# Kernel tuning notes

Measured on AMD Instinct MI355X. Metric: run time of the kernel, lower is better.

## Reference

```python
import jax, jax.numpy as jnp
import numpy as np

K = 3          # kernel_size
PAD = 1        # padding
FOCAL = 50.0
DMIN = 1.0
DMAX = 50.0
ORIG_H = 512.0  # original_image_size[1]


def setup_inputs() -> dict:
    key = jax.random.key(0)
    k1, k2 = jax.random.split(key)
    x = jax.random.normal(k1, (4, 64, 256, 256), dtype=jnp.float32)
    # conv weight [out_ch, in_ch, K, K] (bias=False)
    W = jax.random.normal(k2, (64, 64, K, K), dtype=jnp.float32) * 0.05
    return {"x": x, "W": W}


def _bilinear(img, xs, ys):
    """Bilinear sample img [B,C,H,W] at float pixel coords xs, ys [B,Ho,Wo].
    Zero padding outside the image (grid_sample semantics)."""
    B, C, H, Wd = img.shape
    Ho, Wo = xs.shape[1], xs.shape[2]
    x0 = jnp.floor(xs); y0 = jnp.floor(ys)
    wx1 = xs - x0; wx0 = 1.0 - wx1
    wy1 = ys - y0; wy0 = 1.0 - wy1
    img_flat = img.reshape(B, C, H * Wd)

    def gat(ix, iy):
        ixi = ix.astype(jnp.int32); iyi = iy.astype(jnp.int32)
        valid = (ixi >= 0) & (ixi < Wd) & (iyi >= 0) & (iyi < H)
        idx = jnp.clip(iyi, 0, H - 1) * Wd + jnp.clip(ixi, 0, Wd - 1)
        v = jnp.take_along_axis(img_flat, idx.reshape(B, 1, Ho * Wo), axis=2)
        v = v.reshape(B, C, Ho, Wo)
        return v * valid[:, None].astype(img.dtype)

    return (gat(x0, y0) * (wx0 * wy0)[:, None]
            + gat(x0 + 1, y0) * (wx1 * wy0)[:, None]
            + gat(x0, y0 + 1) * (wx0 * wy1)[:, None]
            + gat(x0 + 1, y0 + 1) * (wx1 * wy1)[:, None])


def reference(x, W):
    B, C, H, Wd = x.shape
    downsample = ORIG_H / H  # 2.0 for H=256

    # upper branch: plain 3x3 conv, padding 1, no bias
    x_upper = jax.lax.conv_general_dilated(x, W, (1, 1), [(PAD, PAD), (PAD, PAD)])

    # geometry -> clamped depth (geometry_method='max', formulation='depth')
    depth = jnp.clip(jnp.max(x, axis=1), DMIN, DMAX)  # [B,H,W]

    # Frontal homography: Hom01 = I with [1,2] = focal/(downsample*depth);
    # its inverse Hom10 shifts y by -s.
    s = FOCAL / (downsample * depth)  # [B,H,W]

    xi = jnp.arange(Wd, dtype=x.dtype)[None, None, :]
    yi = jnp.arange(H, dtype=x.dtype)[None, :, None]
    xs = jnp.broadcast_to(xi, (B, H, Wd))
    ys = yi - s  # Hom10 applied to pixel coords

    # warp input with per-pixel Hom10 (pass_warped_images=True)
    x2 = _bilinear(x, xs, ys)

    # deformable conv: per-pixel offset from Hom10 is (dx,dy)=(0,-s) for all 9 taps
    x_lower = jnp.zeros_like(x_upper)
    for ky in range(K):
        for kx in range(K):
            sx = xs + (kx - PAD)
            sy = ys + (ky - PAD)
            tap = _bilinear(x2, sx, sy)  # [B,C,H,W]
            x_lower = x_lower + jnp.einsum('bchw,oc->bohw', tap, W[:, :, ky, kx])

    # project with 'min' over the stacked (upper, lower) branches
    return jnp.minimum(x_upper, x_lower)
```

## Files before the change

kernel.cpp:

```cpp
#include <hip/hip_runtime.h>
#include <cmath>

constexpr int BB = 4, CC = 64, HH = 256, WW = 256;
constexpr int WP = 258;
constexpr int C2R = 257;

typedef short short8 __attribute__((ext_vector_type(8)));
typedef float f32x4 __attribute__((ext_vector_type(4)));
#define MFMA_BF16 __builtin_amdgcn_mfma_f32_16x16x32_bf16

union U16x8 { uint4 v; unsigned short h[8]; };
union U16x4 { uint2 v; unsigned short h[4]; };

__device__ inline unsigned short f2bf(float f) {
  unsigned u = __builtin_bit_cast(unsigned, f);
  u += 0x7fffu + ((u >> 16) & 1u);
  return (unsigned short)(u >> 16);
}
__device__ inline unsigned short f2bf_trunc(float f) {
  return (unsigned short)(__builtin_bit_cast(unsigned, f) >> 16);
}
__device__ inline float bf2f(unsigned short h) {
  unsigned u = ((unsigned)h) << 16;
  return __builtin_bit_cast(float, u);
}

__global__ __launch_bounds__(256, 4) void k_pack(const float* __restrict__ x,
                                                 float* __restrict__ s,
                                                 unsigned short* __restrict__ xn) {
  __shared__ float tile[CC * 129];
  __shared__ float pmax[2][128];
  const int t = threadIdx.x;
  const int half = blockIdx.x & 1, y = blockIdx.x >> 1, b = blockIdx.y;
  const int px0 = half * 128;
  const int pxl = t & 127, chb = (t >> 7) * 32;

  const float* base = x + (size_t)b * CC * HH * WW + (size_t)y * WW + px0 + pxl;
  float m = -1e30f;
#pragma unroll 8
  for (int i = 0; i < 32; ++i) {
    float v = base[(size_t)(chb + i) * HH * WW];
    tile[(chb + i) * 129 + pxl] = v;
    m = fmaxf(m, v);
  }
  pmax[t >> 7][pxl] = m;

  uint4* xn4 = (uint4*)xn;
  if (t < 8) {
    int col = half ? (WP - 1) : 0;
    xn4[(((size_t)(b * HH + y) * WP + col) * CC + t * 8) >> 3] =
        make_uint4(0, 0, 0, 0);
  }
  __syncthreads();

  if (t < 128) {
    float mm = fmaxf(pmax[0][t], pmax[1][t]);
    s[(b * HH + y) * WW + px0 + t] = 25.0f / fminf(fmaxf(mm, 1.0f), 50.0f);
  }
#pragma unroll
  for (int g = 0; g < 4; ++g) {
    int px = g * 32 + (t >> 3), c8 = t & 7;
    U16x8 r;
#pragma unroll
    for (int j = 0; j < 8; ++j) r.h[j] = f2bf(tile[(c8 * 8 + j) * 129 + px]);
    xn4[(((size_t)(b * HH + y) * WP + px0 + px + 1) * CC + c8 * 8) >> 3] = r.v;
  }
}

__global__ __launch_bounds__(256) void k_wpack(const float* __restrict__ Wt,
                                               unsigned short* __restrict__ Wp) {
  int gid = blockIdx.x * 256 + threadIdx.x;
  int lane = gid & 63, kc = (gid >> 6) & 1, mt = (gid >> 7) & 3, tap = gid >> 9;
  int o = mt * 16 + (lane & 15);
  int kb = kc * 32 + (lane >> 4) * 8;
  int ky = tap / 3, kx = tap % 3;
  U16x8 r;
#pragma unroll
  for (int j = 0; j < 8; ++j)
    r.h[j] = f2bf(Wt[o * 576 + (kb + j) * 9 + ky * 3 + kx]);
  ((uint4*)Wp)[gid] = r.v;
}

__global__ __launch_bounds__(256, 4) void k_lower(const unsigned short* __restrict__ xn,
                                                  const unsigned short* __restrict__ Wp,
                                                  const float* __restrict__ s,
                                                  unsigned short* __restrict__ c2) {
  __shared__ uint4 lds[2112];
  const int t = threadIdx.x;
  const int ctile = blockIdx.x & 3, tr = blockIdx.x >> 2;
  const int b = blockIdx.y;
  const int r0 = tr * 2 - 1;
  const int colBase = ctile * 64;

  const uint4* xn4 = (const uint4*)xn;
#pragma unroll 1
  for (int g = 0; g < 3; ++g) {
    float w0a[3], w1a[3];
    int o0a[3], o1a[3], la[3];
    bool act[3], va[3];
#pragma unroll
    for (int j = 0; j < 3; ++j) {
      int idx = (g * 3 + j) * 256 + t;
      act[j] = idx < 2112;
      int rr_ = idx / 528, rem = idx % 528;
      int col_ = rem >> 3, ch_ = rem & 7;
      int xrow = r0 - 1 + rr_;
      va[j] = act[j] && (xrow >= 0) && (xrow < HH);
      la[j] = (rr_ * 66 + col_) * 8 + (ch_ ^ (col_ & 7));
      float sv = 0.0f;
      int pxc = min(max(colBase + col_ - 1, 0), WW - 1);
      if (va[j]) sv = s[(b * HH + min(max(xrow, 0), HH - 1)) * WW + pxc];
      float ys = (float)xrow - sv;
      float fy = floorf(ys);
      float wfr = ys - fy;
      int i0 = (int)fy;
      w0a[j] = (i0 >= 0) ? 1.0f - wfr : 0.0f;
      w1a[j] = (i0 + 1 >= 0) ? wfr : 0.0f;
      int a0 = min(max(i0, 0), HH - 1), a1 = min(max(i0 + 1, 0), HH - 1);
      o0a[j] = ((b * HH + a0) * WP + colBase + col_) * 8 + ch_;
      o1a[j] = ((b * HH + a1) * WP + colBase + col_) * 8 + ch_;
    }
#pragma unroll
    for (int j = 0; j < 3; ++j) {
      if (act[j]) {
        uint4 v = make_uint4(0, 0, 0, 0);
        if (va[j]) {
          U16x8 u0, u1, rr;
          u0.v = xn4[o0a[j]];
          u1.v = xn4[o1a[j]];
#pragma unroll
          for (int k = 0; k < 8; ++k)
            rr.h[k] = f2bf_trunc(w0a[j] * bf2f(u0.h[k]) + w1a[j] * bf2f(u1.h[k]));
          v = rr.v;
        }
        lds[la[j]] = v;
      }
    }
  }

  const int lane = t & 63, w = t >> 6;
  const int ow = w & 1, ch2 = w >> 1;
  const int quad = lane >> 4, l15 = lane & 15;
  const uint4* wp4 = (const uint4*)Wp;
  __syncthreads();

  f32x4 acc[2][2][2];
#pragma unroll
  for (int pt = 0; pt < 2; ++pt)
#pragma unroll
    for (int rr = 0; rr < 2; ++rr)
#pragma unroll
      for (int ct = 0; ct < 2; ++ct) acc[pt][rr][ct] = {0.f, 0.f, 0.f, 0.f};

#pragma unroll 1
  for (int kc = 0; kc < 2; ++kc) {
    short8 wf[9][2];
#pragma unroll
    for (int tap = 0; tap < 9; ++tap)
#pragma unroll
      for (int ct = 0; ct < 2; ++ct)
        wf[tap][ct] = __builtin_bit_cast(
            short8, wp4[((tap * 4 + (ow * 2 + ct)) * 2 + kc) * 64 + lane]);
#pragma unroll
    for (int pt = 0; pt < 2; ++pt) {
#pragma unroll
      for (int ir = 0; ir < 4; ++ir) {
#pragma unroll
        for (int kx = 0; kx < 3; ++kx) {
          int col = ch2 * 32 + pt * 16 + l15 + kx;
          short8 xf = __builtin_bit_cast(
              short8, lds[(ir * 66 + col) * 8 + ((kc * 4 + quad) ^ (col & 7))]);
          if (ir <= 2) {
#pragma unroll
            for (int ct = 0; ct < 2; ++ct)
              acc[pt][0][ct] = MFMA_BF16(wf[ir * 3 + kx][ct], xf, acc[pt][0][ct], 0, 0, 0);
          }
          if (ir >= 1) {
#pragma unroll
            for (int ct = 0; ct < 2; ++ct)
              acc[pt][1][ct] = MFMA_BF16(wf[(ir - 1) * 3 + kx][ct], xf, acc[pt][1][ct], 0, 0, 0);
          }
        }
      }
    }
  }

  uint2* c2u = (uint2*)c2;
#pragma unroll
  for (int pt = 0; pt < 2; ++pt) {
    int px = colBase + ch2 * 32 + pt * 16 + l15;
#pragma unroll
    for (int rr = 0; rr < 2; ++rr) {
      int r = r0 + rr;
      if (r > 255) continue;
#pragma unroll
      for (int ct = 0; ct < 2; ++ct) {
        f32x4 A = acc[pt][rr][ct];
        int og = (ow * 2 + ct) * 4 + quad;
        unsigned short h0 = f2bf(A[0]), h1 = f2bf(A[1]), h2 = f2bf(A[2]), h3 = f2bf(A[3]);
        uint2 val = make_uint2((unsigned)h0 | ((unsigned)h1 << 16),
                               (unsigned)h2 | ((unsigned)h3 << 16));
        c2u[(size_t)((b * 16 + og) * C2R + (r + 1)) * WW + px] = val;
      }
    }
  }
}

__global__ __launch_bounds__(256, 4) void k_final(const unsigned short* __restrict__ xn,
                                                  const unsigned short* __restrict__ Wp,
                                                  const float* __restrict__ s,
                                                  const unsigned short* __restrict__ c2,
                                                  float* __restrict__ out) {
  __shared__ uint4 lds[2112];
  const int t = threadIdx.x;
  const int ctile = blockIdx.x & 3, tr = blockIdx.x >> 2;
  const int b = blockIdx.y;
  const int y0 = tr * 2;
  const int colBase = ctile * 64;

  const uint4* src4 = (const uint4*)xn;
#pragma unroll 1
  for (int i = 0; i < 9; ++i) {
    int idx = i * 256 + t;
    if (idx < 2112) {
      int rr_ = idx / 528, rem = idx % 528;
      int col_ = rem >> 3, ch_ = rem & 7;
      int xrow = y0 - 1 + rr_;
      uint4 v = make_uint4(0, 0, 0, 0);
      if (xrow >= 0 && xrow < HH)
        v = src4[((size_t)(b * HH + xrow) * WP + colBase + col_) * 8 + ch_];
      lds[(rr_ * 66 + col_) * 8 + (ch_ ^ (col_ & 7))] = v;
    }
  }

  const int lane = t & 63, w = t >> 6;
  const int ow = w & 1, ch2 = w >> 1;
  const int quad = lane >> 4, l15 = lane & 15;
  const uint4* wp4 = (const uint4*)Wp;
  __syncthreads();

  f32x4 acc[2][2][2];
#pragma unroll
  for (int pt = 0; pt < 2; ++pt)
#pragma unroll
    for (int rr = 0; rr < 2; ++rr)
#pragma unroll
      for (int ct = 0; ct < 2; ++ct) acc[pt][rr][ct] = {0.f, 0.f, 0.f, 0.f};

#pragma unroll 1
  for (int kc = 0; kc < 2; ++kc) {
    short8 wf[9][2];
#pragma unroll
    for (int tap = 0; tap < 9; ++tap)
#pragma unroll
      for (int ct = 0; ct < 2; ++ct)
        wf[tap][ct] = __builtin_bit_cast(
            short8, wp4[((tap * 4 + (ow * 2 + ct)) * 2 + kc) * 64 + lane]);
#pragma unroll
    for (int pt = 0; pt < 2; ++pt) {
#pragma unroll
      for (int ir = 0; ir < 4; ++ir) {
#pragma unroll
        for (int kx = 0; kx < 3; ++kx) {
          int col = ch2 * 32 + pt * 16 + l15 + kx;
          short8 xf = __builtin_bit_cast(
              short8, lds[(ir * 66 + col) * 8 + ((kc * 4 + quad) ^ (col & 7))]);
          if (ir <= 2) {
#pragma unroll
            for (int ct = 0; ct < 2; ++ct)
              acc[pt][0][ct] = MFMA_BF16(wf[ir * 3 + kx][ct], xf, acc[pt][0][ct], 0, 0, 0);
          }
          if (ir >= 1) {
#pragma unroll
            for (int ct = 0; ct < 2; ++ct)
              acc[pt][1][ct] = MFMA_BF16(wf[(ir - 1) * 3 + kx][ct], xf, acc[pt][1][ct], 0, 0, 0);
          }
        }
      }
    }
  }

  const uint2* c2u = (const uint2*)c2;
#pragma unroll
  for (int pt = 0; pt < 2; ++pt) {
    int px = colBase + ch2 * 32 + pt * 16 + l15;
#pragma unroll
    for (int rr = 0; rr < 2; ++rr) {
      int y = y0 + rr;
      float sv = s[(b * HH + y) * WW + px];
      float ys = (float)y - sv;
      float fy = floorf(ys);
      float wfr = ys - fy;
      int i0 = (int)fy;
      float lw0 = (i0 + 1 >= 0 && i0 + 1 <= HH) ? 1.0f - wfr : 0.0f;
      float lw1 = (i0 + 2 >= 0 && i0 + 2 <= HH) ? wfr : 0.0f;
      int a0 = min(max(i0 + 1, 0), HH);
      int a1 = min(max(i0 + 2, 0), HH);
#pragma unroll
      for (int ct = 0; ct < 2; ++ct) {
        f32x4 A = acc[pt][rr][ct];
        int og = (ow * 2 + ct) * 4 + quad;
        U16x4 v0, v1;
        v0.v = c2u[(size_t)((b * 16 + og) * C2R + a0) * WW + px];
        v1.v = c2u[(size_t)((b * 16 + og) * C2R + a1) * WW + px];
#pragma unroll
        for (int reg = 0; reg < 4; ++reg) {
          float lower = lw0 * bf2f(v0.h[reg]) + lw1 * bf2f(v1.h[reg]);
          out[((size_t)(b * CC + og * 4 + reg) * HH + y) * WW + px] =
              fminf(A[reg], lower);
        }
      }
    }
  }
}

extern "C" void kernel_launch(void* const* d_in, const int* in_sizes, int n_in,
                              void* d_out, int out_size, void* d_ws, size_t ws_size,
                              hipStream_t stream) {
  const float* x = (const float*)d_in[0];
  const float* Wt = (const float*)d_in[1];
  float* out = (float*)d_out;

  char* ws = (char*)d_ws;
  float* s = (float*)ws;
  unsigned short* Wp = (unsigned short*)(ws + 1048576);
  unsigned short* xn = (unsigned short*)(ws + 1122304);
  unsigned short* c2 = (unsigned short*)(ws + 34938880);
  k_pack<<<dim3(HH * 2, BB), 256, 0, stream>>>(x, s, xn);
  k_wpack<<<dim3(18), 256, 0, stream>>>(Wt, Wp);
  k_lower<<<dim3(4 * 129, BB), 256, 0, stream>>>(xn, Wp, s, c2);
  k_final<<<dim3(4 * 128, BB), 256, 0, stream>>>(xn, Wp, s, c2, out);
}
```

Measured before the change: 189.1 us.

## Fold weight packing into pack kernel, batch gathers, use direct global-to-LDS loads

Weight packing moves into k_pack, which removes one kernel launch. In k_lower, all s values are preloaded and the bilinear source loads are batched ahead of the blend, so more memory requests are in flight at once. In k_final, interior tiles fill LDS with global_load_lds direct copies, applying the XOR swizzle on the source address. The epilogue s reads are hoisted before the main loop. The costs are more register pressure and a separate boundary path for edge tiles.

```diff
diff --git a/kernel.cpp b/kernel.cpp
--- a/kernel.cpp
+++ b/kernel.cpp
@@ -8,6 +8,9 @@
 typedef short short8 __attribute__((ext_vector_type(8)));
 typedef float f32x4 __attribute__((ext_vector_type(4)));
 #define MFMA_BF16 __builtin_amdgcn_mfma_f32_16x16x32_bf16
+
+typedef __attribute__((address_space(1))) const unsigned gptr_t;
+typedef __attribute__((address_space(3))) unsigned lptr_t;
 
 union U16x8 { uint4 v; unsigned short h[8]; };
 union U16x4 { uint2 v; unsigned short h[4]; };
@@ -26,14 +29,29 @@
 }
 
 __global__ __launch_bounds__(256, 4) void k_pack(const float* __restrict__ x,
+                                                 const float* __restrict__ Wt,
                                                  float* __restrict__ s,
-                                                 unsigned short* __restrict__ xn) {
+                                                 unsigned short* __restrict__ xn,
+                                                 unsigned short* __restrict__ Wp) {
   __shared__ float tile[CC * 129];
   __shared__ float pmax[2][128];
   const int t = threadIdx.x;
   const int half = blockIdx.x & 1, y = blockIdx.x >> 1, b = blockIdx.y;
   const int px0 = half * 128;
   const int pxl = t & 127, chb = (t >> 7) * 32;
+
+  if (b == 0 && blockIdx.x < 18) {
+    int gid = blockIdx.x * 256 + t;
+    int lane = gid & 63, kc = (gid >> 6) & 1, mt = (gid >> 7) & 3, tap = gid >> 9;
+    int o = mt * 16 + (lane & 15);
+    int kb = kc * 32 + (lane >> 4) * 8;
+    int ky = tap / 3, kx = tap % 3;
+    U16x8 r;
+#pragma unroll
+    for (int j = 0; j < 8; ++j)
+      r.h[j] = f2bf(Wt[o * 576 + (kb + j) * 9 + ky * 3 + kx]);
+    ((uint4*)Wp)[gid] = r.v;
+  }
 
   const float* base = x + (size_t)b * CC * HH * WW + (size_t)y * WW + px0 + pxl;
   float m = -1e30f;
@@ -65,20 +83,6 @@
     for (int j = 0; j < 8; ++j) r.h[j] = f2bf(tile[(c8 * 8 + j) * 129 + px]);
     xn4[(((size_t)(b * HH + y) * WP + px0 + px + 1) * CC + c8 * 8) >> 3] = r.v;
   }
-}
-
-__global__ __launch_bounds__(256) void k_wpack(const float* __restrict__ Wt,
-                                               unsigned short* __restrict__ Wp) {
-  int gid = blockIdx.x * 256 + threadIdx.x;
-  int lane = gid & 63, kc = (gid >> 6) & 1, mt = (gid >> 7) & 3, tap = gid >> 9;
-  int o = mt * 16 + (lane & 15);
-  int kb = kc * 32 + (lane >> 4) * 8;
-  int ky = tap / 3, kx = tap % 3;
-  U16x8 r;
-#pragma unroll
-  for (int j = 0; j < 8; ++j)
-    r.h[j] = f2bf(Wt[o * 576 + (kb + j) * 9 + ky * 3 + kx]);
-  ((uint4*)Wp)[gid] = r.v;
 }
 
 __global__ __launch_bounds__(256, 4) void k_lower(const unsigned short* __restrict__ xn,
@@ -93,44 +97,65 @@
   const int colBase = ctile * 64;
 
   const uint4* xn4 = (const uint4*)xn;
-#pragma unroll 1
-  for (int g = 0; g < 3; ++g) {
-    float w0a[3], w1a[3];
-    int o0a[3], o1a[3], la[3];
-    bool act[3], va[3];
-#pragma unroll
-    for (int j = 0; j < 3; ++j) {
-      int idx = (g * 3 + j) * 256 + t;
-      act[j] = idx < 2112;
+
+  float sva[9];
+#pragma unroll
+  for (int j = 0; j < 9; ++j) {
+    int idx = j * 256 + t;
+    bool act = (j < 8) || (t < 64);
+    int rr_ = idx / 528, rem = idx % 528;
+    int col_ = rem >> 3;
+    int xrow = r0 - 1 + rr_;
+    bool va = act && (xrow >= 0) && (xrow < HH);
+    int pxc = min(max(colBase + col_ - 1, 0), WW - 1);
+    sva[j] = va ? s[(b * HH + min(max(xrow, 0), HH - 1)) * WW + pxc] : 0.0f;
+  }
+
+#pragma unroll
+  for (int h = 0; h < 2; ++h) {
+    const int jb = h * 5;
+    const int n = h ? 4 : 5;
+    uint4 u0[5], u1[5];
+    float w0a[5], w1a[5];
+    int la[5];
+    bool act[5], va[5];
+#pragma unroll
+    for (int j = 0; j < 5; ++j) {
+      if (j >= n) break;
+      const int e = jb + j;
+      int idx = e * 256 + t;
+      act[j] = (e < 8) || (t < 64);
       int rr_ = idx / 528, rem = idx % 528;
       int col_ = rem >> 3, ch_ = rem & 7;
       int xrow = r0 - 1 + rr_;
       va[j] = act[j] && (xrow >= 0) && (xrow < HH);
       la[j] = (rr_ * 66 + col_) * 8 + (ch_ ^ (col_ & 7));
-      float sv = 0.0f;
-      int pxc = min(max(colBase + col_ - 1, 0), WW - 1);
-      if (va[j]) sv = s[(b * HH + min(max(xrow, 0), HH - 1)) * WW + pxc];
-      float ys = (float)xrow - sv;
+      float ys = (float)xrow - sva[e];
       float fy = floorf(ys);
       float wfr = ys - fy;
       int i0 = (int)fy;
       w0a[j] = (i0 >= 0) ? 1.0f - wfr : 0.0f;
       w1a[j] = (i0 + 1 >= 0) ? wfr : 0.0f;
       int a0 = min(max(i0, 0), HH - 1), a1 = min(max(i0 + 1, 0), HH - 1);
-      o0a[j] = ((b * HH + a0) * WP + colBase + col_) * 8 + ch_;
-      o1a[j] = ((b * HH + a1) * WP + colBase + col_) * 8 + ch_;
-    }
-#pragma unroll
-    for (int j = 0; j < 3; ++j) {
+      int o0 = ((b * HH + a0) * WP + colBase + col_) * 8 + ch_;
+      int o1 = ((b * HH + a1) * WP + colBase + col_) * 8 + ch_;
+      if (va[j]) {
+        u0[j] = xn4[o0];
+        u1[j] = xn4[o1];
+      }
+    }
+#pragma unroll
+    for (int j = 0; j < 5; ++j) {
+      if (j >= n) break;
       if (act[j]) {
         uint4 v = make_uint4(0, 0, 0, 0);
         if (va[j]) {
-          U16x8 u0, u1, rr;
-          u0.v = xn4[o0a[j]];
-          u1.v = xn4[o1a[j]];
+          U16x8 a, bb, rr;
+          a.v = u0[j];
+          bb.v = u1[j];
 #pragma unroll
           for (int k = 0; k < 8; ++k)
-            rr.h[k] = f2bf_trunc(w0a[j] * bf2f(u0.h[k]) + w1a[j] * bf2f(u1.h[k]));
+            rr.h[k] = f2bf_trunc(w0a[j] * bf2f(a.h[k]) + w1a[j] * bf2f(bb.h[k]));
           v = rr.v;
         }
         lds[la[j]] = v;
@@ -218,25 +243,59 @@
   const int y0 = tr * 2;
   const int colBase = ctile * 64;
 
+  const int lane = t & 63, w = t >> 6;
+  const int ow = w & 1, ch2 = w >> 1;
+  const int quad = lane >> 4, l15 = lane & 15;
   const uint4* src4 = (const uint4*)xn;
-#pragma unroll 1
-  for (int i = 0; i < 9; ++i) {
-    int idx = i * 256 + t;
-    if (idx < 2112) {
+  const uint4* wp4 = (const uint4*)Wp;
+
+  float sv_e[2][2];
+#pragma unroll
+  for (int pt = 0; pt < 2; ++pt)
+#pragma unroll
+    for (int rr = 0; rr < 2; ++rr)
+      sv_e[pt][rr] =
+          s[(b * HH + (y0 + rr)) * WW + (colBase + ch2 * 32 + pt * 16 + l15)];
+
+  if (tr > 0 && tr < 127) {
+#pragma unroll
+    for (int i = 0; i < 8; ++i) {
+      int idx = i * 256 + t;
       int rr_ = idx / 528, rem = idx % 528;
       int col_ = rem >> 3, ch_ = rem & 7;
       int xrow = y0 - 1 + rr_;
-      uint4 v = make_uint4(0, 0, 0, 0);
-      if (xrow >= 0 && xrow < HH)
-        v = src4[((size_t)(b * HH + xrow) * WP + colBase + col_) * 8 + ch_];
-      lds[(rr_ * 66 + col_) * 8 + (ch_ ^ (col_ & 7))] = v;
-    }
-  }
-
-  const int lane = t & 63, w = t >> 6;
-  const int ow = w & 1, ch2 = w >> 1;
-  const int quad = lane >> 4, l15 = lane & 15;
-  const uint4* wp4 = (const uint4*)Wp;
+      size_t srcIdx =
+          ((size_t)(b * HH + xrow) * WP + colBase + col_) * 8 + (ch_ ^ (col_ & 7));
+      __builtin_amdgcn_global_load_lds((gptr_t*)(const void*)(src4 + srcIdx),
+                                       (lptr_t*)(void*)&lds[i * 256 + (t & 192)],
+                                       16, 0, 0);
+    }
+    if (t < 64) {
+      int idx = 2048 + t;
+      int rr_ = idx / 528, rem = idx % 528;
+      int col_ = rem >> 3, ch_ = rem & 7;
+      int xrow = y0 - 1 + rr_;
+      size_t srcIdx =
+          ((size_t)(b * HH + xrow) * WP + colBase + col_) * 8 + (ch_ ^ (col_ & 7));
+      __builtin_amdgcn_global_load_lds((gptr_t*)(const void*)(src4 + srcIdx),
+                                       (lptr_t*)(void*)&lds[2048],
+                                       16, 0, 0);
+    }
+  } else {
+#pragma unroll
+    for (int i = 0; i < 9; ++i) {
+      int idx = i * 256 + t;
+      if (idx < 2112) {
+        int rr_ = idx / 528, rem = idx % 528;
+        int col_ = rem >> 3, ch_ = rem & 7;
+        int xrow = y0 - 1 + rr_;
+        uint4 v = make_uint4(0, 0, 0, 0);
+        if (xrow >= 0 && xrow < HH)
+          v = src4[((size_t)(b * HH + xrow) * WP + colBase + col_) * 8 + ch_];
+        lds[(rr_ * 66 + col_) * 8 + (ch_ ^ (col_ & 7))] = v;
+      }
+    }
+  }
   __syncthreads();
 
   f32x4 acc[2][2][2];
@@ -287,7 +346,7 @@
 #pragma unroll
     for (int rr = 0; rr < 2; ++rr) {
       int y = y0 + rr;
-      float sv = s[(b * HH + y) * WW + px];
+      float sv = sv_e[pt][rr];
       float ys = (float)y - sv;
       float fy = floorf(ys);
       float wfr = ys - fy;
@@ -326,8 +385,7 @@
   unsigned short* Wp = (unsigned short*)(ws + 1048576);
   unsigned short* xn = (unsigned short*)(ws + 1122304);
   unsigned short* c2 = (unsigned short*)(ws + 34938880);
-  k_pack<<<dim3(HH * 2, BB), 256, 0, stream>>>(x, s, xn);
-  k_wpack<<<dim3(18), 256, 0, stream>>>(Wt, Wp);
+  k_pack<<<dim3(HH * 2, BB), 256, 0, stream>>>(x, Wt, s, xn, Wp);
   k_lower<<<dim3(4 * 129, BB), 256, 0, stream>>>(xn, Wp, s, c2);
   k_final<<<dim3(4 * 128, BB), 256, 0, stream>>>(xn, Wp, s, c2, out);
 }
```

After: 187.9 us. Within noise of the previous version (-0.7%).
